# Performance work log

Hardware: AMD Instinct MI355X
Metric: run time of the kernel (lower is better)

## Reference

```python
import jax, jax.numpy as jnp
import numpy as np

INNER = 256   # inner_channel
NODES = 64    # nodes_num (prototypes)
EM_NUM = 3
DIAG_C = 128  # hardcoded diag_channel in FullyConnectGCLayer


def setup_inputs() -> dict:
    key = jax.random.key(0)
    ks = jax.random.split(key, 16)
    b, c, w, h = 4, 1024, 64, 64
    f32 = jnp.float32
    d = {}
    d["x"] = jax.random.normal(ks[0], (b, c, w, h), f32)
    # Conv2d weights re-initialized to N(0, 0.001) in Intra_graph.__init__
    d["W_in"] = 0.001 * jax.random.normal(ks[1], (INNER, c), f32)
    d["b_in"] = jnp.zeros((INNER,), f32)
    d["multi_proto"] = 0.001 * jax.random.normal(ks[2], (1, INNER, NODES), f32)
    d["pi0"] = jnp.ones((1, NODES), f32) / NODES
    # Conv1d layers keep default kaiming-uniform-ish init
    lim = 1.0 / np.sqrt(INNER)
    d["W_adj"] = jax.random.uniform(ks[3], (DIAG_C, INNER), f32, -lim, lim)
    d["b_adj"] = jax.random.uniform(ks[4], (DIAG_C,), f32, -lim, lim)
    d["W_diag"] = jax.random.uniform(ks[5], (DIAG_C, INNER), f32, -lim, lim)
    d["b_diag"] = jax.random.uniform(ks[6], (DIAG_C,), f32, -lim, lim)
    d["gcn_weight"] = 0.01 * jax.random.normal(ks[7], (INNER, INNER), f32)
    d["W_out"] = 0.001 * jax.random.normal(ks[8], (c, INNER), f32)
    d["b_out"] = jnp.zeros((c,), f32)
    d["gamma"] = jnp.ones((c,), f32)
    d["beta"] = jnp.zeros((c,), f32)
    d["W_out2"] = 0.001 * jax.random.normal(ks[9], (c, INNER), f32)
    d["b_out2"] = jnp.zeros((c,), f32)
    d["gamma2"] = jnp.ones((c,), f32)
    d["beta2"] = jnp.zeros((c,), f32)
    d["flag"] = 0
    return d


def _bn(y, g, bt):
    # BatchNorm2d in training mode: batch stats over (N,H,W), biased var, eps=1e-5
    m = jnp.mean(y, (0, 2, 3), keepdims=True)
    v = jnp.var(y, (0, 2, 3), keepdims=True)
    return (y - m) * jax.lax.rsqrt(v + 1e-5) * g[None, :, None, None] + bt[None, :, None, None]


def _forward(x, W_in, b_in, multi_proto, pi0, W_adj, b_adj, W_diag, b_diag,
             gcn_weight, W_out, b_out, gamma, beta, W_out2, b_out2, gamma2, beta2):
    b, c, w, h = x.shape
    wh = w * h
    x1 = (jnp.einsum('oi,bihw->bohw', W_in, x) + b_in[None, :, None, None]).reshape(b, INNER, wh)
    # ---- EM soft-clustering loop (runs under no_grad in torch) ----
    x1s = jax.lax.stop_gradient(x1)
    mu = jnp.broadcast_to(multi_proto, (b, INNER, NODES))
    pi = jnp.broadcast_to(pi0[None, :, :], (b, 1, NODES))
    for _ in range(EM_NUM):
        lik = jnp.einsum('bcm,bcn->bmn', x1s, mu)              # [b, wh, n]
        lik = jnp.exp(lik - jnp.max(lik, 2, keepdims=True))
        post = lik * pi
        post = post / (1e-18 + jnp.sum(post, 2, keepdims=True))
        prob = post / (1e-18 + jnp.sum(post, 1, keepdims=True))
        mu = jnp.einsum('bcm,bmn->bcn', x1s, prob)
        pi = jnp.sum(post, 1, keepdims=True) / wh
    post = jax.lax.stop_gradient(post)
    prob = jax.lax.stop_gradient(prob)
    # ---- aggregate to prototypes (grad flows through x1 only) ----
    x2 = jnp.einsum('bcm,bmn->bcn', x1, prob)                   # [b, inner, n]
    # ---- branch 2: scatter back, conv, bn ----
    x4 = jnp.einsum('bcn,bmn->bcm', x2, post).reshape(b, INNER, w, h)
    x4 = _bn(jnp.einsum('oi,bihw->bohw', W_out2, x4) + b_out2[None, :, None, None], gamma2, beta2)
    output2 = jax.nn.relu(jax.nn.relu(x4) + x)
    # ---- FullyConnectGCLayer on x2 ----
    xd = jnp.einsum('oi,bin->bon', W_diag, x2) + b_diag[None, :, None]
    dvec = jax.nn.sigmoid(jnp.mean(xd, 2))                      # [b, 128]
    xa = jnp.einsum('oi,bin->bon', W_adj, x2) + b_adj[None, :, None]  # [b, 128, n]
    # sigmoid(diag(d)) has 0.5 off-diagonal, sigmoid(d) on diagonal:
    # xa^T S xa = 0.5 * (1^T xa)^T (1^T xa) + xa^T diag(sig(d)-0.5) xa
    u = jnp.sum(xa, 1)                                          # [b, n]
    A = 0.5 * u[:, :, None] * u[:, None, :] + jnp.einsum('bcn,bc,bcm->bnm', xa, dvec - 0.5, xa)
    A = jax.nn.relu(A) + jnp.eye(NODES, dtype=x.dtype)[None]
    deg = jax.lax.stop_gradient(jnp.sum(A, 1) ** -0.5)          # no_grad degree, [b, n]
    A = deg[:, :, None] * A * deg[:, None, :]
    gout = jnp.einsum('oi,bin->bon', gcn_weight, jnp.einsum('bcn,bnm->bcm', x2, A))
    x2g = jax.nn.relu(gout) + x2                                # res_connect
    # ---- branch 1: scatter back, conv, bn ----
    x3 = jnp.einsum('bcn,bmn->bcm', x2g, post).reshape(b, INNER, w, h)
    x3 = _bn(jnp.einsum('oi,bihw->bohw', W_out, x3) + b_out[None, :, None, None], gamma, beta)
    output = jax.nn.relu(jax.nn.relu(x3) + x)
    return output, output2


def reference(x, W_in, b_in, multi_proto, pi0, W_adj, b_adj, W_diag, b_diag,
              gcn_weight, W_out, b_out, gamma, beta, W_out2, b_out2, gamma2, beta2, flag):
    # flag only gates a buffer EMA update (no effect on forward outputs)
    return _forward(x, W_in, b_in, multi_proto, pi0, W_adj, b_adj, W_diag, b_diag,
                    gcn_weight, W_out, b_out, gamma, beta, W_out2, b_out2, gamma2, beta2)
```

## Files before the change

kernel.cpp:

```cpp
#include <hip/hip_runtime.h>
#include <math.h>


typedef unsigned short u16;
typedef short s16x8 __attribute__((ext_vector_type(8)));
typedef float f32x4 __attribute__((ext_vector_type(4)));

constexpr int BB  = 4;
constexpr int CH  = 1024;
constexpr int IN  = 256;
constexpr int ND  = 64;
constexpr int WH  = 4096;
constexpr int DCN = 128;
constexpr size_t TOT = (size_t)BB * CH * WH;

__device__ inline u16 f2bf(float f) {
  unsigned u = __float_as_uint(f);
  return (u16)((u + 0x7fffu + ((u >> 16) & 1u)) >> 16);
}
__device__ inline s16x8 ld8(const u16* p) { return *(const s16x8*)p; }
#define MFMA16(a, b, c) __builtin_amdgcn_mfma_f32_16x16x32_bf16(a, b, c, 0, 0, 0)

__global__ void k_init(const float* __restrict__ Win, const float* __restrict__ mp,
                       const float* __restrict__ pi0, u16* __restrict__ Winb,
                       u16* __restrict__ mu_t, float* __restrict__ piw,
                       float* __restrict__ sp) {
  int idx = blockIdx.x * 256 + threadIdx.x;
  if (idx < IN * CH) { Winb[idx] = f2bf(Win[idx]); return; }
  int j = idx - IN * CH;
  if (j < BB * ND * IN) {
    int bb = j >> 14, n = (j >> 8) & 63, c = j & 255;
    mu_t[((size_t)(bb * ND + n)) * IN + c] = f2bf(mp[c * ND + n]);
    return;
  }
  j -= BB * ND * IN;
  if (j < BB * ND) { piw[j] = pi0[j & 63]; return; }
  j -= BB * ND;
  if (j < 3 * BB * ND) sp[j] = 0.f;
}

__global__ __launch_bounds__(512) void k_x1(
    const float* __restrict__ x, const u16* __restrict__ Winb,
    const float* __restrict__ bin, u16* __restrict__ x1, u16* __restrict__ x1t) {
  __shared__ u16 lt[64][40];
  const int t = threadIdx.x, w = t >> 6, lr = t & 15, lg = (t >> 4) & 3;
  const int wc = w & 3, wm = w >> 2;
  const int m0 = blockIdx.x * 64, b = blockIdx.y;
  const int si = t >> 4, sm = (t & 15) * 4;
  const float* xb = x + (size_t)b * CH * WH + m0 + sm;
  f32x4 acc[4][2];
#pragma unroll
  for (int i = 0; i < 4; ++i)
#pragma unroll
    for (int j = 0; j < 2; ++j) acc[i][j] = (f32x4){0.f, 0.f, 0.f, 0.f};
  const u16* wp = Winb + (size_t)(wc * 64 + lr) * CH + lg * 8;

  float4 nxt = *(const float4*)&xb[(size_t)si * WH];
  for (int k0 = 0; k0 < CH; k0 += 32) {
    float4 cur = nxt;
    __syncthreads();
    lt[sm + 0][si] = f2bf(cur.x); lt[sm + 1][si] = f2bf(cur.y);
    lt[sm + 2][si] = f2bf(cur.z); lt[sm + 3][si] = f2bf(cur.w);
    if (k0 + 32 < CH) nxt = *(const float4*)&xb[(size_t)(k0 + 32 + si) * WH];
    __syncthreads();
    s16x8 af[4], bf[2];
#pragma unroll
    for (int i = 0; i < 4; ++i) af[i] = ld8(wp + (size_t)i * 16 * CH + k0);
#pragma unroll
    for (int j = 0; j < 2; ++j) bf[j] = *(const s16x8*)&lt[wm * 32 + j * 16 + lr][lg * 8];
#pragma unroll
    for (int i = 0; i < 4; ++i)
#pragma unroll
      for (int j = 0; j < 2; ++j) acc[i][j] = MFMA16(af[i], bf[j], acc[i][j]);
  }
#pragma unroll
  for (int i = 0; i < 4; ++i) {
    const int cb = wc * 64 + i * 16 + lg * 4;
    const float4 bi = *(const float4*)&bin[cb];
    const float bia[4] = {bi.x, bi.y, bi.z, bi.w};
#pragma unroll
    for (int j = 0; j < 2; ++j) {
      const int m = m0 + wm * 32 + j * 16 + lr;
      float v[4];
#pragma unroll
      for (int r = 0; r < 4; ++r) v[r] = acc[i][j][r] + bia[r];
      ushort4 o;
      o.x = f2bf(v[0]); o.y = f2bf(v[1]); o.z = f2bf(v[2]); o.w = f2bf(v[3]);
      *(ushort4*)&x1t[((size_t)b * WH + m) * IN + cb] = o;
#pragma unroll
      for (int r = 0; r < 4; ++r)
        x1[((size_t)b * IN + cb + r) * WH + m] = f2bf(v[r]);
    }
  }
}

__global__ __launch_bounds__(256) void k_em(
    const u16* __restrict__ x1, const u16* __restrict__ x1t,
    const u16* __restrict__ mu_t, const float* __restrict__ piw,
    float* __restrict__ sp, u16* __restrict__ pmn,
    float* __restrict__ mup, float* __restrict__ gp, int doLast) {
  __shared__ u16 ptl[64][264];
  const int t = threadIdx.x, w = t >> 6, lr = t & 15, lg = (t >> 4) & 3;
  const int mch = blockIdx.x, b = blockIdx.y;
  const int mbase = mch * 256;
  {
    f32x4 acc[4][4];
#pragma unroll
    for (int i = 0; i < 4; ++i)
#pragma unroll
      for (int f = 0; f < 4; ++f) acc[i][f] = (f32x4){0.f, 0.f, 0.f, 0.f};
    const u16* ap = x1t + ((size_t)b * WH + mbase + w * 64 + lr) * IN + lg * 8;
    const u16* bp = mu_t + ((size_t)b * ND + lr) * IN + lg * 8;
#pragma unroll
    for (int k0 = 0; k0 < IN; k0 += 32) {
      s16x8 bf[4];
#pragma unroll
      for (int f = 0; f < 4; ++f) bf[f] = ld8(bp + f * 16 * IN + k0);
#pragma unroll
      for (int i = 0; i < 4; ++i) {
        s16x8 av = ld8(ap + (size_t)i * 16 * IN + k0);
#pragma unroll
        for (int f = 0; f < 4; ++f) acc[i][f] = MFMA16(av, bf[f], acc[i][f]);
      }
    }
    float pi_[4], spart[4] = {0.f, 0.f, 0.f, 0.f};
#pragma unroll
    for (int f = 0; f < 4; ++f) pi_[f] = piw[b * ND + f * 16 + lr];
#pragma unroll
    for (int i = 0; i < 4; ++i)
#pragma unroll
      for (int r = 0; r < 4; ++r) {
        float v0 = acc[i][0][r], v1 = acc[i][1][r], v2 = acc[i][2][r], v3 = acc[i][3][r];
        float mx = fmaxf(fmaxf(v0, v1), fmaxf(v2, v3));
        mx = fmaxf(mx, __shfl_xor(mx, 1)); mx = fmaxf(mx, __shfl_xor(mx, 2));
        mx = fmaxf(mx, __shfl_xor(mx, 4)); mx = fmaxf(mx, __shfl_xor(mx, 8));
        float e0 = __expf(v0 - mx) * pi_[0], e1 = __expf(v1 - mx) * pi_[1];
        float e2 = __expf(v2 - mx) * pi_[2], e3 = __expf(v3 - mx) * pi_[3];
        float s = e0 + e1 + e2 + e3;
        s += __shfl_xor(s, 1); s += __shfl_xor(s, 2);
        s += __shfl_xor(s, 4); s += __shfl_xor(s, 8);
        const float inv = 1.f / (1e-18f + s);
        e0 *= inv; e1 *= inv; e2 *= inv; e3 *= inv;
        const int mloc = w * 64 + i * 16 + lg * 4 + r;
        u16 q0 = f2bf(e0), q1 = f2bf(e1), q2 = f2bf(e2), q3 = f2bf(e3);
        ptl[0 + lr][mloc]  = q0; ptl[16 + lr][mloc] = q1;
        ptl[32 + lr][mloc] = q2; ptl[48 + lr][mloc] = q3;
        if (doLast) {
          const size_t gbase = ((size_t)b * WH + mbase + mloc) * ND + lr;
          pmn[gbase + 0]  = q0; pmn[gbase + 16] = q1;
          pmn[gbase + 32] = q2; pmn[gbase + 48] = q3;
        }
        spart[0] += e0; spart[1] += e1; spart[2] += e2; spart[3] += e3;
      }
#pragma unroll
    for (int f = 0; f < 4; ++f) {
      spart[f] += __shfl_xor(spart[f], 16);
      spart[f] += __shfl_xor(spart[f], 32);
    }
    if (((t >> 4) & 3) == 0) {
#pragma unroll
      for (int f = 0; f < 4; ++f)
        atomicAdd(&sp[b * ND + f * 16 + lr], spart[f]);
    }
  }
  __syncthreads();
  {
    f32x4 acc[4][4];
#pragma unroll
    for (int i = 0; i < 4; ++i)
#pragma unroll
      for (int j = 0; j < 4; ++j) acc[i][j] = (f32x4){0.f, 0.f, 0.f, 0.f};
    const u16* ap = x1 + ((size_t)b * IN + w * 64 + lr) * WH + mbase + lg * 8;
#pragma unroll
    for (int ks = 0; ks < 8; ++ks) {
      s16x8 af[4], bf[4];
#pragma unroll
      for (int i = 0; i < 4; ++i) af[i] = ld8(ap + (size_t)i * 16 * WH + ks * 32);
#pragma unroll
      for (int j = 0; j < 4; ++j)
        bf[j] = *(const s16x8*)&ptl[j * 16 + lr][ks * 32 + lg * 8];
#pragma unroll
      for (int i = 0; i < 4; ++i)
#pragma unroll
        for (int j = 0; j < 4; ++j) acc[i][j] = MFMA16(af[i], bf[j], acc[i][j]);
    }
    float* mo = mup + ((size_t)mch * BB + b) * (IN * ND);
#pragma unroll
    for (int i = 0; i < 4; ++i)
#pragma unroll
      for (int j = 0; j < 4; ++j)
#pragma unroll
        for (int r = 0; r < 4; ++r) {
          const int c = w * 64 + i * 16 + lg * 4 + r, n = j * 16 + lr;
          mo[c * ND + n] = acc[i][j][r];
        }
  }
  if (doLast) {
    f32x4 acc[4];
#pragma unroll
    for (int j = 0; j < 4; ++j) acc[j] = (f32x4){0.f, 0.f, 0.f, 0.f};
#pragma unroll
    for (int ks = 0; ks < 8; ++ks) {
      s16x8 av = *(const s16x8*)&ptl[w * 16 + lr][ks * 32 + lg * 8];
#pragma unroll
      for (int j = 0; j < 4; ++j) {
        s16x8 bq = *(const s16x8*)&ptl[j * 16 + lr][ks * 32 + lg * 8];
        acc[j] = MFMA16(av, bq, acc[j]);
      }
    }
    float* go = gp + ((size_t)mch * BB + b) * (ND * ND);
#pragma unroll
    for (int j = 0; j < 4; ++j)
#pragma unroll
      for (int r = 0; r < 4; ++r) {
        const int n1 = w * 16 + lg * 4 + r, n2 = j * 16 + lr;
        go[n1 * ND + n2] = acc[j][r];
      }
  }
}

__global__ void k_mu_red(const float* __restrict__ mup, const float* __restrict__ spb,
                         float* __restrict__ piw, float* __restrict__ mu,
                         u16* __restrict__ mu_t, const float* __restrict__ gp,
                         float* __restrict__ G, int doG) {
  const int idx = blockIdx.x * 256 + threadIdx.x;
  const int bb = idx >> 14, c = (idx >> 6) & 255, n = idx & 63;
  float s = 0.f;
#pragma unroll
  for (int ch = 0; ch < 16; ++ch)
    s += mup[((size_t)ch * BB + bb) * (IN * ND) + (idx & 16383)];
  const float v = s / (1e-18f + spb[bb * ND + n]);
  mu[idx] = v;
  mu_t[((size_t)(bb * ND + n)) * IN + c] = f2bf(v);
  if (idx < BB * ND) piw[idx] = spb[idx] * (1.f / (float)WH);
  if (doG && idx < BB * ND * ND) {
    float g = 0.f;
#pragma unroll
    for (int ch = 0; ch < 16; ++ch) g += gp[(size_t)ch * (BB * ND * ND) + idx];
    G[idx] = g;
  }
}

__device__ void zg_body(const float* __restrict__ W, const float* __restrict__ v,
                        float* __restrict__ z, u16* __restrict__ zb,
                        int o0, int bb, int t, char* smem) {
  float (*As)[68] = (float(*)[68])smem;
  float (*Bs)[64] = (float(*)[64])(smem + 4352);
  const int tx = t & 15, ty = t >> 4;
  const int aoo = t >> 2, akq = (t & 3) * 4;
  const int bkk = t >> 4, bnq = (t & 15) * 4;
  float acc[4][4] = {};
  for (int k0 = 0; k0 < IN; k0 += 16) {
    {
      float4 w4 = *(const float4*)&W[(size_t)(o0 + aoo) * IN + k0 + akq];
      As[akq + 0][aoo] = w4.x; As[akq + 1][aoo] = w4.y;
      As[akq + 2][aoo] = w4.z; As[akq + 3][aoo] = w4.w;
    }
    *(float4*)&Bs[bkk][bnq] = *(const float4*)&v[((size_t)bb * IN + k0 + bkk) * ND + bnq];
    __syncthreads();
#pragma unroll
    for (int kk = 0; kk < 16; ++kk) {
      float4 a4 = *(const float4*)&As[kk][ty * 4];
      float4 b4 = *(const float4*)&Bs[kk][tx * 4];
      float ar[4] = {a4.x, a4.y, a4.z, a4.w}, br[4] = {b4.x, b4.y, b4.z, b4.w};
#pragma unroll
      for (int i = 0; i < 4; ++i)
#pragma unroll
        for (int j = 0; j < 4; ++j) acc[i][j] += ar[i] * br[j];
    }
    __syncthreads();
  }
#pragma unroll
  for (int i = 0; i < 4; ++i) {
    float4 r = make_float4(acc[i][0], acc[i][1], acc[i][2], acc[i][3]);
    const size_t off = ((size_t)bb * CH + o0 + ty * 4 + i) * ND + tx * 4;
    *(float4*)&z[off] = r;
    ushort4 h;
    h.x = f2bf(r.x); h.y = f2bf(r.y); h.z = f2bf(r.z); h.w = f2bf(r.w);
    *(ushort4*)&zb[off] = h;
  }
}

__global__ __launch_bounds__(256) void k_gcAz2(
    const float* __restrict__ mu, const float* __restrict__ gw,
    const float* __restrict__ Wa, const float* __restrict__ ba,
    const float* __restrict__ Wd, const float* __restrict__ bd,
    float* __restrict__ qbuf, float* __restrict__ xabuf, float* __restrict__ dv,
    const float* __restrict__ Wo2, float* __restrict__ z2, u16* __restrict__ zb2) {
  __shared__ __align__(16) char smem[66560];
  const int t = threadIdx.x, bid = blockIdx.x;
  if (bid < 28) {
    const int blk = bid % 7, b = bid / 7;
    float* sx2 = (float*)smem;
    float* srm = (float*)(smem + 65536);
    if (blk < 6) {
      const float* src = mu + (size_t)b * IN * ND;
#pragma unroll
      for (int q4 = 0; q4 < 16; ++q4)
        *(float4*)&sx2[q4 * 1024 + t * 4] = *(const float4*)&src[q4 * 1024 + t * 4];
      __syncthreads();
      const int rg = t >> 4, cg2 = t & 15;
      const float* W = (blk < 4) ? gw + (size_t)(blk * 64 + rg * 4) * IN
                                 : Wa + (size_t)((blk - 4) * 64 + rg * 4) * IN;
      float acc[4][4] = {};
      for (int i4 = 0; i4 < 64; ++i4) {
        float4 xv[4];
#pragma unroll
        for (int e = 0; e < 4; ++e)
          xv[e] = *(const float4*)&sx2[(i4 * 4 + e) * 64 + cg2 * 4];
#pragma unroll
        for (int rr = 0; rr < 4; ++rr) {
          const float4 w4 = *(const float4*)&W[(size_t)rr * IN + i4 * 4];
          acc[rr][0] += w4.x * xv[0].x + w4.y * xv[1].x + w4.z * xv[2].x + w4.w * xv[3].x;
          acc[rr][1] += w4.x * xv[0].y + w4.y * xv[1].y + w4.z * xv[2].y + w4.w * xv[3].y;
          acc[rr][2] += w4.x * xv[0].z + w4.y * xv[1].z + w4.z * xv[2].z + w4.w * xv[3].z;
          acc[rr][3] += w4.x * xv[0].w + w4.y * xv[1].w + w4.z * xv[2].w + w4.w * xv[3].w;
        }
      }
      if (blk < 4) {
        float* dst = qbuf + (size_t)b * IN * ND + (size_t)(blk * 64 + rg * 4) * ND + cg2 * 4;
#pragma unroll
        for (int rr = 0; rr < 4; ++rr)
          *(float4*)&dst[(size_t)rr * ND] =
              make_float4(acc[rr][0], acc[rr][1], acc[rr][2], acc[rr][3]);
      } else {
        const int xr = (blk - 4) * 64 + rg * 4;
        float* dst = xabuf + (size_t)b * DCN * ND + (size_t)xr * ND + cg2 * 4;
#pragma unroll
        for (int rr = 0; rr < 4; ++rr) {
          const float bv = ba[xr + rr];
          *(float4*)&dst[(size_t)rr * ND] =
              make_float4(acc[rr][0] + bv, acc[rr][1] + bv, acc[rr][2] + bv, acc[rr][3] + bv);
        }
      }
    } else {
      {
        const float* row = mu + (size_t)b * IN * ND + (size_t)t * ND;
        float s = 0.f;
#pragma unroll
        for (int n4 = 0; n4 < 16; ++n4) {
          float4 v = *(const float4*)&row[n4 * 4];
          s += v.x + v.y + v.z + v.w;
        }
        srm[t] = s * (1.f / ND);
      }
      __syncthreads();
      if (t < DCN) {
        float av = 0.f;
#pragma unroll
        for (int i4 = 0; i4 < 64; ++i4) {
          float4 w4 = *(const float4*)&Wd[(size_t)t * IN + i4 * 4];
          float4 r4 = *(const float4*)&srm[i4 * 4];
          av += w4.x * r4.x + w4.y * r4.y + w4.z * r4.z + w4.w * r4.w;
        }
        av += bd[t];
        dv[b * DCN + t] = 1.f / (1.f + __expf(-av)) - 0.5f;
      }
    }
  } else if (bid >= 32 && bid < 96) {
    const int zid = bid - 32;
    zg_body(Wo2, mu, z2, zb2, (zid & 15) * 64, zid >> 4, t, smem);
  }
}

__global__ __launch_bounds__(256) void k_gcBC(
    const float* __restrict__ xabuf, const float* __restrict__ dv,
    const float* __restrict__ qbuf, const float* __restrict__ mu,
    float* __restrict__ x2g) {
  __shared__ float sxa[DCN * ND];
  __shared__ float sA[ND * 65];
  __shared__ float sq[64 * 68];
  __shared__ float sdv[DCN];
  __shared__ float su[ND];
  __shared__ float sdeg[ND];
  const int t = threadIdx.x, qtr = blockIdx.x, b = blockIdx.y;
  {
    const float* src = xabuf + (size_t)b * DCN * ND;
#pragma unroll
    for (int q4 = 0; q4 < 8; ++q4)
      *(float4*)&sxa[q4 * 1024 + t * 4] = *(const float4*)&src[q4 * 1024 + t * 4];
    if (t < DCN) sdv[t] = dv[b * DCN + t];
    const int r = t >> 2, seg = (t & 3) * 16;
    const float* qs = qbuf + (size_t)b * IN * ND + (size_t)(qtr * 64 + r) * ND + seg;
#pragma unroll
    for (int f = 0; f < 4; ++f) {
      float4 v = *(const float4*)&qs[f * 4];
      sq[r * 68 + seg + f * 4 + 0] = v.x; sq[r * 68 + seg + f * 4 + 1] = v.y;
      sq[r * 68 + seg + f * 4 + 2] = v.z; sq[r * 68 + seg + f * 4 + 3] = v.w;
    }
  }
  __syncthreads();
  if (t < ND) {
    float s = 0.f;
    for (int dc = 0; dc < DCN; ++dc) s += sxa[dc * ND + t];
    su[t] = s;
  }
  __syncthreads();
  {
    const int n1g = t >> 4, n2g = t & 15;
    float acc[4][4] = {};
    for (int dc = 0; dc < DCN; ++dc) {
      const float dvv = sdv[dc];
      float4 v1 = *(const float4*)&sxa[dc * ND + n1g * 4];
      const float4 v2 = *(const float4*)&sxa[dc * ND + n2g * 4];
      v1.x *= dvv; v1.y *= dvv; v1.z *= dvv; v1.w *= dvv;
      acc[0][0] += v1.x * v2.x; acc[0][1] += v1.x * v2.y;
      acc[0][2] += v1.x * v2.z; acc[0][3] += v1.x * v2.w;
      acc[1][0] += v1.y * v2.x; acc[1][1] += v1.y * v2.y;
      acc[1][2] += v1.y * v2.z; acc[1][3] += v1.y * v2.w;
      acc[2][0] += v1.z * v2.x; acc[2][1] += v1.z * v2.y;
      acc[2][2] += v1.z * v2.z; acc[2][3] += v1.z * v2.w;
      acc[3][0] += v1.w * v2.x; acc[3][1] += v1.w * v2.y;
      acc[3][2] += v1.w * v2.z; acc[3][3] += v1.w * v2.w;
    }
#pragma unroll
    for (int i = 0; i < 4; ++i) {
      const int n1 = n1g * 4 + i;
      const float u1 = su[n1];
#pragma unroll
      for (int j = 0; j < 4; ++j) {
        const int n2 = n2g * 4 + j;
        const float v = acc[i][j] + 0.5f * u1 * su[n2];
        sA[n1 * 65 + n2] = fmaxf(v, 0.f) + (n1 == n2 ? 1.f : 0.f);
      }
    }
  }
  __syncthreads();
  if (t < ND) {
    float s = 0.f;
    for (int m = 0; m < ND; ++m) s += sA[m * 65 + t];
    sdeg[t] = rsqrtf(s);
  }
  __syncthreads();
  {
    const int n1g = t >> 4, n2g = t & 15;
#pragma unroll
    for (int i = 0; i < 4; ++i) {
      const int n1 = n1g * 4 + i;
      const float dr = sdeg[n1];
#pragma unroll
      for (int e = 0; e < 4; ++e)
        sA[n1 * 65 + n2g * 4 + e] *= dr * sdeg[n2g * 4 + e];
    }
  }
  __syncthreads();
  {
    const int rg = t >> 4, cg2 = t & 15;
    float acc[4][4] = {};
    for (int k = 0; k < ND; ++k) {
      const float4 a4 = *(const float4*)&sA[k * 65 + cg2 * 4];
      float qv[4];
#pragma unroll
      for (int rr = 0; rr < 4; ++rr) qv[rr] = sq[(rg * 4 + rr) * 68 + k];
#pragma unroll
      for (int rr = 0; rr < 4; ++rr) {
        acc[rr][0] += qv[rr] * a4.x; acc[rr][1] += qv[rr] * a4.y;
        acc[rr][2] += qv[rr] * a4.z; acc[rr][3] += qv[rr] * a4.w;
      }
    }
#pragma unroll
    for (int rr = 0; rr < 4; ++rr) {
      const size_t off = (size_t)b * IN * ND + (size_t)(qtr * 64 + rg * 4 + rr) * ND + cg2 * 4;
      const float4 xv = *(const float4*)&mu[off];
      float4 o;
      o.x = fmaxf(acc[rr][0], 0.f) + xv.x; o.y = fmaxf(acc[rr][1], 0.f) + xv.y;
      o.z = fmaxf(acc[rr][2], 0.f) + xv.z; o.w = fmaxf(acc[rr][3], 0.f) + xv.w;
      *(float4*)&x2g[off] = o;
    }
  }
}

__global__ __launch_bounds__(256) void k_zg(
    const float* __restrict__ W, const float* __restrict__ v,
    float* __restrict__ z, u16* __restrict__ zb) {
  __shared__ __align__(16) char smem[8448];
  zg_body(W, v, z, zb, blockIdx.x * 64, blockIdx.y, threadIdx.x, smem);
}

__global__ __launch_bounds__(256) void k_stats(
    const float* __restrict__ z1, const float* __restrict__ z2,
    const float* __restrict__ sp, const float* __restrict__ G,
    const float* __restrict__ gam, const float* __restrict__ bet,
    const float* __restrict__ gam2, const float* __restrict__ bet2,
    float* __restrict__ abc) {
  const int t = threadIdx.x;
  const int o = blockIdx.x * 4 + (t >> 6), lane = t & 63;
#pragma unroll
  for (int br = 0; br < 2; ++br) {
    const float* z = br ? z2 : z1;
    float macc = 0.f, eacc = 0.f;
    for (int bb = 0; bb < BB; ++bb) {
      const float zv = z[((size_t)bb * CH + o) * ND + lane];
      float s1 = zv * sp[bb * ND + lane];
      const float* Gb = G + (size_t)bb * ND * ND;
      float gz = 0.f;
      for (int k = 0; k < ND; ++k) {
        const float zk = __shfl(zv, k);
        gz += Gb[k * ND + lane] * zk;
      }
      float q = zv * gz;
#pragma unroll
      for (int off = 32; off; off >>= 1) {
        s1 += __shfl_xor(s1, off);
        q  += __shfl_xor(q, off);
      }
      macc += s1; eacc += q;
    }
    const float inv = 1.f / (float)((size_t)BB * WH);
    const float mean = macc * inv;
    const float var  = eacc * inv - mean * mean;
    const float a = (br ? gam2[o] : gam[o]) * rsqrtf(var + 1e-5f);
    const float c = (br ? bet2[o] : bet[o]) - mean * a;
    if (lane == 0) { abc[br * 2 * CH + o] = a; abc[br * 2 * CH + CH + o] = c; }
  }
}

__global__ __launch_bounds__(256) void k_epi(
    const u16* __restrict__ zb1, const u16* __restrict__ zb2,
    const u16* __restrict__ post, const float* __restrict__ abc,
    const float* __restrict__ x, float* __restrict__ out1, float* __restrict__ out2) {
  const int t = threadIdx.x, w = t >> 6, lr = t & 15, lg = (t >> 4) & 3;
  const int m0 = blockIdx.x * 256 + w * 64, o0 = blockIdx.y * 64, bb = blockIdx.z;
  f32x4 acc1[4][4], acc2[4][4];
#pragma unroll
  for (int i = 0; i < 4; ++i)
#pragma unroll
    for (int j = 0; j < 4; ++j) {
      acc1[i][j] = (f32x4){0.f, 0.f, 0.f, 0.f};
      acc2[i][j] = (f32x4){0.f, 0.f, 0.f, 0.f};
    }
  const u16* z1p = zb1 + ((size_t)bb * CH + o0 + lr) * ND + lg * 8;
  const u16* z2p = zb2 + ((size_t)bb * CH + o0 + lr) * ND + lg * 8;
  const u16* pp  = post + ((size_t)bb * WH + m0 + lr) * ND + lg * 8;
#pragma unroll
  for (int ks = 0; ks < 2; ++ks) {
    s16x8 a1[4], a2[4], bq[4];
#pragma unroll
    for (int i = 0; i < 4; ++i) {
      a1[i] = ld8(z1p + i * 16 * ND + ks * 32);
      a2[i] = ld8(z2p + i * 16 * ND + ks * 32);
    }
#pragma unroll
    for (int j = 0; j < 4; ++j) bq[j] = ld8(pp + j * 16 * ND + ks * 32);
#pragma unroll
    for (int i = 0; i < 4; ++i)
#pragma unroll
      for (int j = 0; j < 4; ++j) {
        acc1[i][j] = MFMA16(a1[i], bq[j], acc1[i][j]);
        acc2[i][j] = MFMA16(a2[i], bq[j], acc2[i][j]);
      }
  }
#pragma unroll
  for (int i = 0; i < 4; ++i)
#pragma unroll
    for (int r = 0; r < 4; ++r) {
      const int o = o0 + i * 16 + lg * 4 + r;
      const float a1v = abc[o], c1v = abc[CH + o];
      const float a2v = abc[2 * CH + o], c2v = abc[3 * CH + o];
      const size_t base = ((size_t)bb * CH + o) * WH + m0 + lr;
#pragma unroll
      for (int j = 0; j < 4; ++j) {
        const size_t off = base + j * 16;
        const float xv = __builtin_nontemporal_load(&x[off]);
        const float r1 = fmaxf(fmaxf(a1v * acc1[i][j][r] + c1v, 0.f) + xv, 0.f);
        const float r2 = fmaxf(fmaxf(a2v * acc2[i][j][r] + c2v, 0.f) + xv, 0.f);
        __builtin_nontemporal_store(r1, &out1[off]);
        __builtin_nontemporal_store(r2, &out2[off]);
      }
    }
}

extern "C" void kernel_launch(void* const* d_in, const int* in_sizes, int n_in,
                              void* d_out, int out_size, void* d_ws, size_t ws_size,
                              hipStream_t stream) {
  (void)in_sizes; (void)n_in; (void)out_size; (void)ws_size;
  const float* x    = (const float*)d_in[0];
  const float* Win  = (const float*)d_in[1];
  const float* bin  = (const float*)d_in[2];
  const float* mp   = (const float*)d_in[3];
  const float* pi0  = (const float*)d_in[4];
  const float* Wa   = (const float*)d_in[5];
  const float* ba   = (const float*)d_in[6];
  const float* Wd   = (const float*)d_in[7];
  const float* bd   = (const float*)d_in[8];
  const float* gw   = (const float*)d_in[9];
  const float* Wo   = (const float*)d_in[10];
  const float* gam  = (const float*)d_in[12];
  const float* bet  = (const float*)d_in[13];
  const float* Wo2  = (const float*)d_in[14];
  const float* gam2 = (const float*)d_in[16];
  const float* bet2 = (const float*)d_in[17];

  char* ob = (char*)d_out;
  char* wp = (char*)d_ws;
  float* mup = (float*)(ob + 0);
  float* gp  = (float*)(ob + 4194304);
  float* z1  = (float*)(ob + 5242880);
  float* z2  = (float*)(ob + 6291456);
  u16*   x1    = (u16*)(wp + 0);
  u16*   x1t   = (u16*)(wp + 8388608);
  u16*   Winb  = (u16*)(wp + 16777216);
  u16*   mu_t  = (u16*)(wp + 17301504);
  u16*   pmn   = (u16*)(wp + 17432576);
  float* mu    = (float*)(wp + 19529728);
  float* x2g   = (float*)(wp + 19791872);
  u16*   zb1   = (u16*)(wp + 20054016);
  u16*   zb2   = (u16*)(wp + 20578304);
  float* sp3   = (float*)(wp + 21102592);
  float* piw   = (float*)(wp + 21105664);
  float* abc   = (float*)(wp + 21106688);
  float* G     = (float*)(wp + 21123072);
  float* qbuf  = (float*)(wp + 21188608);
  float* xabuf = (float*)(wp + 21450752);
  float* dvb   = (float*)(wp + 21581824);
  float* out1  = (float*)d_out;
  float* out2  = out1 + TOT;

  k_init<<<dim3(1284), 256, 0, stream>>>(Win, mp, pi0, Winb, mu_t, piw, sp3);
  k_x1<<<dim3(64, BB), 512, 0, stream>>>(x, Winb, bin, x1, x1t);
  for (int it = 0; it < 3; ++it) {
    float* spb = sp3 + it * 256;
    const int doLast = (it == 2);
    k_em<<<dim3(16, BB), 256, 0, stream>>>(x1, x1t, mu_t, piw, spb, pmn, mup, gp, doLast);
    k_mu_red<<<dim3(256), 256, 0, stream>>>(mup, spb, piw, mu, mu_t, gp, G, doLast);
  }
  k_gcAz2<<<dim3(96), 256, 0, stream>>>(mu, gw, Wa, ba, Wd, bd, qbuf, xabuf, dvb,
                                        Wo2, z2, zb2);
  k_gcBC<<<dim3(4, BB), 256, 0, stream>>>(xabuf, dvb, qbuf, mu, x2g);
  k_zg<<<dim3(16, BB), 256, 0, stream>>>(Wo, x2g, z1, zb1);
  k_stats<<<dim3(256), 256, 0, stream>>>(z1, z2, sp3 + 512, G, gam, bet, gam2, bet2, abc);
  k_epi<<<dim3(16, 16, BB), 256, 0, stream>>>(zb1, zb2, pmn, abc, x, out1, out2);
}
```

Measured before the change: 276.5 us.

## Fuse EM mu reduction into k_em via atomics and spread over more blocks

Removes the separate k_mu_red kernel. k_em now accumulates mu and G directly with float atomics into per-iteration buffers, and the next iteration or the downstream kernels apply the 1/sum normalisation on load. The EM grid grows from 16x4 to 64x4 blocks with 64-pixel chunks, and mu is staged in LDS as bf16 inside each block, so occupancy should rise and three launches disappear. In exchange there are many more global float atomics (each block adds a 256x64 tile), summation order becomes nondeterministic, and the normalisation is recomputed redundantly in several consumers.

```diff
diff --git a/kernel.cpp b/kernel.cpp
--- a/kernel.cpp
+++ b/kernel.cpp
@@ -22,21 +22,18 @@
 #define MFMA16(a, b, c) __builtin_amdgcn_mfma_f32_16x16x32_bf16(a, b, c, 0, 0, 0)
 
 __global__ void k_init(const float* __restrict__ Win, const float* __restrict__ mp,
-                       const float* __restrict__ pi0, u16* __restrict__ Winb,
-                       u16* __restrict__ mu_t, float* __restrict__ piw,
-                       float* __restrict__ sp) {
+                       u16* __restrict__ Winb, float* __restrict__ macc,
+                       float* __restrict__ spbuf, float* __restrict__ G) {
   int idx = blockIdx.x * 256 + threadIdx.x;
   if (idx < IN * CH) { Winb[idx] = f2bf(Win[idx]); return; }
   int j = idx - IN * CH;
-  if (j < BB * ND * IN) {
-    int bb = j >> 14, n = (j >> 8) & 63, c = j & 255;
-    mu_t[((size_t)(bb * ND + n)) * IN + c] = f2bf(mp[c * ND + n]);
-    return;
-  }
-  j -= BB * ND * IN;
-  if (j < BB * ND) { piw[j] = pi0[j & 63]; return; }
-  j -= BB * ND;
-  if (j < 3 * BB * ND) sp[j] = 0.f;
+  if (j < BB * IN * ND) { macc[j] = mp[j & (IN * ND - 1)]; return; }
+  j -= BB * IN * ND;
+  if (j < 3 * BB * IN * ND) { macc[BB * IN * ND + j] = 0.f; return; }
+  j -= 3 * BB * IN * ND;
+  if (j < 4 * BB * ND) { spbuf[j] = 0.f; return; }
+  j -= 4 * BB * ND;
+  if (j < BB * ND * ND) G[j] = 0.f;
 }
 
 __global__ __launch_bounds__(512) void k_x1(
@@ -96,62 +93,74 @@
 
 __global__ __launch_bounds__(256) void k_em(
     const u16* __restrict__ x1, const u16* __restrict__ x1t,
-    const u16* __restrict__ mu_t, const float* __restrict__ piw,
-    float* __restrict__ sp, u16* __restrict__ pmn,
-    float* __restrict__ mup, float* __restrict__ gp, int doLast) {
-  __shared__ u16 ptl[64][264];
+    const float* __restrict__ maccPrev, const float* __restrict__ spPrev,
+    const float* __restrict__ pi0, float* __restrict__ maccNext,
+    float* __restrict__ spNext, u16* __restrict__ pmn, float* __restrict__ G,
+    int it0, int doLast) {
+  __shared__ u16 lt_mu[64][264];
+  __shared__ u16 ptl[64][72];
   const int t = threadIdx.x, w = t >> 6, lr = t & 15, lg = (t >> 4) & 3;
   const int mch = blockIdx.x, b = blockIdx.y;
-  const int mbase = mch * 256;
   {
-    f32x4 acc[4][4];
-#pragma unroll
-    for (int i = 0; i < 4; ++i)
-#pragma unroll
-      for (int f = 0; f < 4; ++f) acc[i][f] = (f32x4){0.f, 0.f, 0.f, 0.f};
-    const u16* ap = x1t + ((size_t)b * WH + mbase + w * 64 + lr) * IN + lg * 8;
-    const u16* bp = mu_t + ((size_t)b * ND + lr) * IN + lg * 8;
+    const int n0 = (t * 4) & 63;
+    float inv[4];
+#pragma unroll
+    for (int e = 0; e < 4; ++e)
+      inv[e] = it0 ? 1.f : 1.f / (1e-18f + spPrev[b * ND + n0 + e]);
+    const float* src = maccPrev + (size_t)b * (IN * ND);
+#pragma unroll
+    for (int q = 0; q < 16; ++q) {
+      const int idx = q * 1024 + t * 4;
+      const int c = idx >> 6;
+      float4 v = *(const float4*)&src[idx];
+      lt_mu[n0 + 0][c] = f2bf(v.x * inv[0]);
+      lt_mu[n0 + 1][c] = f2bf(v.y * inv[1]);
+      lt_mu[n0 + 2][c] = f2bf(v.z * inv[2]);
+      lt_mu[n0 + 3][c] = f2bf(v.w * inv[3]);
+    }
+  }
+  __syncthreads();
+  {
+    f32x4 acc[4];
+#pragma unroll
+    for (int f = 0; f < 4; ++f) acc[f] = (f32x4){0.f, 0.f, 0.f, 0.f};
+    const u16* ap = x1t + ((size_t)b * WH + mch * 64 + w * 16 + lr) * IN + lg * 8;
 #pragma unroll
     for (int k0 = 0; k0 < IN; k0 += 32) {
-      s16x8 bf[4];
-#pragma unroll
-      for (int f = 0; f < 4; ++f) bf[f] = ld8(bp + f * 16 * IN + k0);
-#pragma unroll
-      for (int i = 0; i < 4; ++i) {
-        s16x8 av = ld8(ap + (size_t)i * 16 * IN + k0);
-#pragma unroll
-        for (int f = 0; f < 4; ++f) acc[i][f] = MFMA16(av, bf[f], acc[i][f]);
-      }
+      s16x8 av = ld8(ap + k0);
+#pragma unroll
+      for (int f = 0; f < 4; ++f)
+        acc[f] = MFMA16(av, *(const s16x8*)&lt_mu[f * 16 + lr][lg * 8 + k0], acc[f]);
     }
     float pi_[4], spart[4] = {0.f, 0.f, 0.f, 0.f};
 #pragma unroll
-    for (int f = 0; f < 4; ++f) pi_[f] = piw[b * ND + f * 16 + lr];
-#pragma unroll
-    for (int i = 0; i < 4; ++i)
-#pragma unroll
-      for (int r = 0; r < 4; ++r) {
-        float v0 = acc[i][0][r], v1 = acc[i][1][r], v2 = acc[i][2][r], v3 = acc[i][3][r];
-        float mx = fmaxf(fmaxf(v0, v1), fmaxf(v2, v3));
-        mx = fmaxf(mx, __shfl_xor(mx, 1)); mx = fmaxf(mx, __shfl_xor(mx, 2));
-        mx = fmaxf(mx, __shfl_xor(mx, 4)); mx = fmaxf(mx, __shfl_xor(mx, 8));
-        float e0 = __expf(v0 - mx) * pi_[0], e1 = __expf(v1 - mx) * pi_[1];
-        float e2 = __expf(v2 - mx) * pi_[2], e3 = __expf(v3 - mx) * pi_[3];
-        float s = e0 + e1 + e2 + e3;
-        s += __shfl_xor(s, 1); s += __shfl_xor(s, 2);
-        s += __shfl_xor(s, 4); s += __shfl_xor(s, 8);
-        const float inv = 1.f / (1e-18f + s);
-        e0 *= inv; e1 *= inv; e2 *= inv; e3 *= inv;
-        const int mloc = w * 64 + i * 16 + lg * 4 + r;
-        u16 q0 = f2bf(e0), q1 = f2bf(e1), q2 = f2bf(e2), q3 = f2bf(e3);
-        ptl[0 + lr][mloc]  = q0; ptl[16 + lr][mloc] = q1;
-        ptl[32 + lr][mloc] = q2; ptl[48 + lr][mloc] = q3;
-        if (doLast) {
-          const size_t gbase = ((size_t)b * WH + mbase + mloc) * ND + lr;
-          pmn[gbase + 0]  = q0; pmn[gbase + 16] = q1;
-          pmn[gbase + 32] = q2; pmn[gbase + 48] = q3;
-        }
-        spart[0] += e0; spart[1] += e1; spart[2] += e2; spart[3] += e3;
-      }
+    for (int f = 0; f < 4; ++f)
+      pi_[f] = it0 ? pi0[f * 16 + lr]
+                   : spPrev[b * ND + f * 16 + lr] * (1.f / (float)WH);
+#pragma unroll
+    for (int r = 0; r < 4; ++r) {
+      float v0 = acc[0][r], v1 = acc[1][r], v2 = acc[2][r], v3 = acc[3][r];
+      float mx = fmaxf(fmaxf(v0, v1), fmaxf(v2, v3));
+      mx = fmaxf(mx, __shfl_xor(mx, 1)); mx = fmaxf(mx, __shfl_xor(mx, 2));
+      mx = fmaxf(mx, __shfl_xor(mx, 4)); mx = fmaxf(mx, __shfl_xor(mx, 8));
+      float e0 = __expf(v0 - mx) * pi_[0], e1 = __expf(v1 - mx) * pi_[1];
+      float e2 = __expf(v2 - mx) * pi_[2], e3 = __expf(v3 - mx) * pi_[3];
+      float s = e0 + e1 + e2 + e3;
+      s += __shfl_xor(s, 1); s += __shfl_xor(s, 2);
+      s += __shfl_xor(s, 4); s += __shfl_xor(s, 8);
+      const float inv = 1.f / (1e-18f + s);
+      e0 *= inv; e1 *= inv; e2 *= inv; e3 *= inv;
+      const int mloc = w * 16 + lg * 4 + r;
+      u16 q0 = f2bf(e0), q1 = f2bf(e1), q2 = f2bf(e2), q3 = f2bf(e3);
+      ptl[0 + lr][mloc]  = q0; ptl[16 + lr][mloc] = q1;
+      ptl[32 + lr][mloc] = q2; ptl[48 + lr][mloc] = q3;
+      if (doLast) {
+        const size_t gbase = ((size_t)b * WH + mch * 64 + mloc) * ND + lr;
+        pmn[gbase + 0]  = q0; pmn[gbase + 16] = q1;
+        pmn[gbase + 32] = q2; pmn[gbase + 48] = q3;
+      }
+      spart[0] += e0; spart[1] += e1; spart[2] += e2; spart[3] += e3;
+    }
 #pragma unroll
     for (int f = 0; f < 4; ++f) {
       spart[f] += __shfl_xor(spart[f], 16);
@@ -160,7 +169,7 @@
     if (((t >> 4) & 3) == 0) {
 #pragma unroll
       for (int f = 0; f < 4; ++f)
-        atomicAdd(&sp[b * ND + f * 16 + lr], spart[f]);
+        atomicAdd(&spNext[b * ND + f * 16 + lr], spart[f]);
     }
   }
   __syncthreads();
@@ -170,9 +179,9 @@
     for (int i = 0; i < 4; ++i)
 #pragma unroll
       for (int j = 0; j < 4; ++j) acc[i][j] = (f32x4){0.f, 0.f, 0.f, 0.f};
-    const u16* ap = x1 + ((size_t)b * IN + w * 64 + lr) * WH + mbase + lg * 8;
-#pragma unroll
-    for (int ks = 0; ks < 8; ++ks) {
+    const u16* ap = x1 + ((size_t)b * IN + w * 64 + lr) * WH + mch * 64 + lg * 8;
+#pragma unroll
+    for (int ks = 0; ks < 2; ++ks) {
       s16x8 af[4], bf[4];
 #pragma unroll
       for (int i = 0; i < 4; ++i) af[i] = ld8(ap + (size_t)i * 16 * WH + ks * 32);
@@ -184,7 +193,7 @@
 #pragma unroll
         for (int j = 0; j < 4; ++j) acc[i][j] = MFMA16(af[i], bf[j], acc[i][j]);
     }
-    float* mo = mup + ((size_t)mch * BB + b) * (IN * ND);
+    float* mo = maccNext + (size_t)b * (IN * ND);
 #pragma unroll
     for (int i = 0; i < 4; ++i)
 #pragma unroll
@@ -192,7 +201,7 @@
 #pragma unroll
         for (int r = 0; r < 4; ++r) {
           const int c = w * 64 + i * 16 + lg * 4 + r, n = j * 16 + lr;
-          mo[c * ND + n] = acc[i][j][r];
+          atomicAdd(&mo[c * ND + n], acc[i][j][r]);
         }
   }
   if (doLast) {
@@ -200,7 +209,7 @@
 #pragma unroll
     for (int j = 0; j < 4; ++j) acc[j] = (f32x4){0.f, 0.f, 0.f, 0.f};
 #pragma unroll
-    for (int ks = 0; ks < 8; ++ks) {
+    for (int ks = 0; ks < 2; ++ks) {
       s16x8 av = *(const s16x8*)&ptl[w * 16 + lr][ks * 32 + lg * 8];
 #pragma unroll
       for (int j = 0; j < 4; ++j) {
@@ -208,47 +217,31 @@
         acc[j] = MFMA16(av, bq, acc[j]);
       }
     }
-    float* go = gp + ((size_t)mch * BB + b) * (ND * ND);
+    float* go = G + (size_t)b * (ND * ND);
 #pragma unroll
     for (int j = 0; j < 4; ++j)
 #pragma unroll
       for (int r = 0; r < 4; ++r) {
         const int n1 = w * 16 + lg * 4 + r, n2 = j * 16 + lr;
-        go[n1 * ND + n2] = acc[j][r];
-      }
-  }
-}
-
-__global__ void k_mu_red(const float* __restrict__ mup, const float* __restrict__ spb,
-                         float* __restrict__ piw, float* __restrict__ mu,
-                         u16* __restrict__ mu_t, const float* __restrict__ gp,
-                         float* __restrict__ G, int doG) {
-  const int idx = blockIdx.x * 256 + threadIdx.x;
-  const int bb = idx >> 14, c = (idx >> 6) & 255, n = idx & 63;
-  float s = 0.f;
-#pragma unroll
-  for (int ch = 0; ch < 16; ++ch)
-    s += mup[((size_t)ch * BB + bb) * (IN * ND) + (idx & 16383)];
-  const float v = s / (1e-18f + spb[bb * ND + n]);
-  mu[idx] = v;
-  mu_t[((size_t)(bb * ND + n)) * IN + c] = f2bf(v);
-  if (idx < BB * ND) piw[idx] = spb[idx] * (1.f / (float)WH);
-  if (doG && idx < BB * ND * ND) {
-    float g = 0.f;
-#pragma unroll
-    for (int ch = 0; ch < 16; ++ch) g += gp[(size_t)ch * (BB * ND * ND) + idx];
-    G[idx] = g;
+        atomicAdd(&go[n1 * ND + n2], acc[j][r]);
+      }
   }
 }
 
 __device__ void zg_body(const float* __restrict__ W, const float* __restrict__ v,
                         float* __restrict__ z, u16* __restrict__ zb,
-                        int o0, int bb, int t, char* smem) {
+                        int o0, int bb, int t, char* smem,
+                        const float* __restrict__ spn) {
   float (*As)[68] = (float(*)[68])smem;
   float (*Bs)[64] = (float(*)[64])(smem + 4352);
   const int tx = t & 15, ty = t >> 4;
   const int aoo = t >> 2, akq = (t & 3) * 4;
   const int bkk = t >> 4, bnq = (t & 15) * 4;
+  float inv4[4] = {1.f, 1.f, 1.f, 1.f};
+  if (spn) {
+#pragma unroll
+    for (int e = 0; e < 4; ++e) inv4[e] = 1.f / (1e-18f + spn[bb * ND + bnq + e]);
+  }
   float acc[4][4] = {};
   for (int k0 = 0; k0 < IN; k0 += 16) {
     {
@@ -256,7 +249,11 @@
       As[akq + 0][aoo] = w4.x; As[akq + 1][aoo] = w4.y;
       As[akq + 2][aoo] = w4.z; As[akq + 3][aoo] = w4.w;
     }
-    *(float4*)&Bs[bkk][bnq] = *(const float4*)&v[((size_t)bb * IN + k0 + bkk) * ND + bnq];
+    {
+      float4 bv = *(const float4*)&v[((size_t)bb * IN + k0 + bkk) * ND + bnq];
+      Bs[bkk][bnq + 0] = bv.x * inv4[0]; Bs[bkk][bnq + 1] = bv.y * inv4[1];
+      Bs[bkk][bnq + 2] = bv.z * inv4[2]; Bs[bkk][bnq + 3] = bv.w * inv4[3];
+    }
     __syncthreads();
 #pragma unroll
     for (int kk = 0; kk < 16; ++kk) {
@@ -282,22 +279,34 @@
 }
 
 __global__ __launch_bounds__(256) void k_gcAz2(
-    const float* __restrict__ mu, const float* __restrict__ gw,
-    const float* __restrict__ Wa, const float* __restrict__ ba,
-    const float* __restrict__ Wd, const float* __restrict__ bd,
-    float* __restrict__ qbuf, float* __restrict__ xabuf, float* __restrict__ dv,
+    const float* __restrict__ macc3, const float* __restrict__ spL,
+    const float* __restrict__ gw, const float* __restrict__ Wa,
+    const float* __restrict__ ba, const float* __restrict__ Wd,
+    const float* __restrict__ bd, float* __restrict__ qbuf,
+    float* __restrict__ xabuf, float* __restrict__ dv,
     const float* __restrict__ Wo2, float* __restrict__ z2, u16* __restrict__ zb2) {
   __shared__ __align__(16) char smem[66560];
   const int t = threadIdx.x, bid = blockIdx.x;
   if (bid < 28) {
     const int blk = bid % 7, b = bid / 7;
-    float* sx2 = (float*)smem;
-    float* srm = (float*)(smem + 65536);
     if (blk < 6) {
-      const float* src = mu + (size_t)b * IN * ND;
-#pragma unroll
-      for (int q4 = 0; q4 < 16; ++q4)
-        *(float4*)&sx2[q4 * 1024 + t * 4] = *(const float4*)&src[q4 * 1024 + t * 4];
+      float* sx2 = (float*)smem;
+      const float* src = macc3 + (size_t)b * IN * ND;
+      {
+        const int n0 = (t * 4) & 63;
+        float inv4[4];
+#pragma unroll
+        for (int e = 0; e < 4; ++e)
+          inv4[e] = 1.f / (1e-18f + spL[b * ND + n0 + e]);
+#pragma unroll
+        for (int q4 = 0; q4 < 16; ++q4) {
+          float4 v = *(const float4*)&src[q4 * 1024 + t * 4];
+          sx2[q4 * 1024 + t * 4 + 0] = v.x * inv4[0];
+          sx2[q4 * 1024 + t * 4 + 1] = v.y * inv4[1];
+          sx2[q4 * 1024 + t * 4 + 2] = v.z * inv4[2];
+          sx2[q4 * 1024 + t * 4 + 3] = v.w * inv4[3];
+        }
+      }
       __syncthreads();
       const int rg = t >> 4, cg2 = t & 15;
       const float* W = (blk < 4) ? gw + (size_t)(blk * 64 + rg * 4) * IN
@@ -334,13 +343,18 @@
         }
       }
     } else {
+      float* sinv = (float*)smem;
+      float* srm  = (float*)(smem + 1024);
+      if (t < ND) sinv[t] = 1.f / (1e-18f + spL[b * ND + t]);
+      __syncthreads();
       {
-        const float* row = mu + (size_t)b * IN * ND + (size_t)t * ND;
+        const float* row = macc3 + (size_t)b * IN * ND + (size_t)t * ND;
         float s = 0.f;
 #pragma unroll
         for (int n4 = 0; n4 < 16; ++n4) {
           float4 v = *(const float4*)&row[n4 * 4];
-          s += v.x + v.y + v.z + v.w;
+          s += v.x * sinv[n4 * 4 + 0] + v.y * sinv[n4 * 4 + 1] +
+               v.z * sinv[n4 * 4 + 2] + v.w * sinv[n4 * 4 + 3];
         }
         srm[t] = s * (1.f / ND);
       }
@@ -359,14 +373,14 @@
     }
   } else if (bid >= 32 && bid < 96) {
     const int zid = bid - 32;
-    zg_body(Wo2, mu, z2, zb2, (zid & 15) * 64, zid >> 4, t, smem);
+    zg_body(Wo2, macc3, z2, zb2, (zid & 15) * 64, zid >> 4, t, smem, spL);
   }
 }
 
 __global__ __launch_bounds__(256) void k_gcBC(
     const float* __restrict__ xabuf, const float* __restrict__ dv,
-    const float* __restrict__ qbuf, const float* __restrict__ mu,
-    float* __restrict__ x2g) {
+    const float* __restrict__ qbuf, const float* __restrict__ macc3,
+    const float* __restrict__ spL, float* __restrict__ x2g) {
   __shared__ float sxa[DCN * ND];
   __shared__ float sA[ND * 65];
   __shared__ float sq[64 * 68];
@@ -446,6 +460,10 @@
   __syncthreads();
   {
     const int rg = t >> 4, cg2 = t & 15;
+    float inv4[4];
+#pragma unroll
+    for (int e = 0; e < 4; ++e)
+      inv4[e] = 1.f / (1e-18f + spL[b * ND + cg2 * 4 + e]);
     float acc[4][4] = {};
     for (int k = 0; k < ND; ++k) {
       const float4 a4 = *(const float4*)&sA[k * 65 + cg2 * 4];
@@ -461,10 +479,12 @@
 #pragma unroll
     for (int rr = 0; rr < 4; ++rr) {
       const size_t off = (size_t)b * IN * ND + (size_t)(qtr * 64 + rg * 4 + rr) * ND + cg2 * 4;
-      const float4 xv = *(const float4*)&mu[off];
+      const float4 xv = *(const float4*)&macc3[off];
       float4 o;
-      o.x = fmaxf(acc[rr][0], 0.f) + xv.x; o.y = fmaxf(acc[rr][1], 0.f) + xv.y;
-      o.z = fmaxf(acc[rr][2], 0.f) + xv.z; o.w = fmaxf(acc[rr][3], 0.f) + xv.w;
+      o.x = fmaxf(acc[rr][0], 0.f) + xv.x * inv4[0];
+      o.y = fmaxf(acc[rr][1], 0.f) + xv.y * inv4[1];
+      o.z = fmaxf(acc[rr][2], 0.f) + xv.z * inv4[2];
+      o.w = fmaxf(acc[rr][3], 0.f) + xv.w * inv4[3];
       *(float4*)&x2g[off] = o;
     }
   }
@@ -474,7 +494,7 @@
     const float* __restrict__ W, const float* __restrict__ v,
     float* __restrict__ z, u16* __restrict__ zb) {
   __shared__ __align__(16) char smem[8448];
-  zg_body(W, v, z, zb, blockIdx.x * 64, blockIdx.y, threadIdx.x, smem);
+  zg_body(W, v, z, zb, blockIdx.x * 64, blockIdx.y, threadIdx.x, smem, nullptr);
 }
 
 __global__ __launch_bounds__(256) void k_stats(
@@ -593,41 +613,40 @@
 
   char* ob = (char*)d_out;
   char* wp = (char*)d_ws;
-  float* mup = (float*)(ob + 0);
-  float* gp  = (float*)(ob + 4194304);
-  float* z1  = (float*)(ob + 5242880);
-  float* z2  = (float*)(ob + 6291456);
+  float* z1 = (float*)(ob + 0);
+  float* z2 = (float*)(ob + 1048576);
   u16*   x1    = (u16*)(wp + 0);
   u16*   x1t   = (u16*)(wp + 8388608);
   u16*   Winb  = (u16*)(wp + 16777216);
-  u16*   mu_t  = (u16*)(wp + 17301504);
-  u16*   pmn   = (u16*)(wp + 17432576);
-  float* mu    = (float*)(wp + 19529728);
-  float* x2g   = (float*)(wp + 19791872);
-  u16*   zb1   = (u16*)(wp + 20054016);
-  u16*   zb2   = (u16*)(wp + 20578304);
-  float* sp3   = (float*)(wp + 21102592);
-  float* piw   = (float*)(wp + 21105664);
-  float* abc   = (float*)(wp + 21106688);
-  float* G     = (float*)(wp + 21123072);
-  float* qbuf  = (float*)(wp + 21188608);
-  float* xabuf = (float*)(wp + 21450752);
-  float* dvb   = (float*)(wp + 21581824);
+  u16*   pmn   = (u16*)(wp + 17301504);
+  float* macc  = (float*)(wp + 19398656);
+  float* spbuf = (float*)(wp + 20447232);
+  float* G     = (float*)(wp + 20451328);
+  float* qbuf  = (float*)(wp + 20516864);
+  float* xabuf = (float*)(wp + 20779008);
+  float* dvb   = (float*)(wp + 20910080);
+  float* x2g   = (float*)(wp + 20912128);
+  u16*   zb1   = (u16*)(wp + 21174272);
+  u16*   zb2   = (u16*)(wp + 21698560);
+  float* abc   = (float*)(wp + 22222848);
   float* out1  = (float*)d_out;
   float* out2  = out1 + TOT;
 
-  k_init<<<dim3(1284), 256, 0, stream>>>(Win, mp, pi0, Winb, mu_t, piw, sp3);
+  float* macc3 = macc + 3 * (BB * IN * ND);
+  float* spL   = spbuf + 3 * (BB * ND);
+
+  k_init<<<dim3(2116), 256, 0, stream>>>(Win, mp, Winb, macc, spbuf, G);
   k_x1<<<dim3(64, BB), 512, 0, stream>>>(x, Winb, bin, x1, x1t);
   for (int it = 0; it < 3; ++it) {
-    float* spb = sp3 + it * 256;
-    const int doLast = (it == 2);
-    k_em<<<dim3(16, BB), 256, 0, stream>>>(x1, x1t, mu_t, piw, spb, pmn, mup, gp, doLast);
-    k_mu_red<<<dim3(256), 256, 0, stream>>>(mup, spb, piw, mu, mu_t, gp, G, doLast);
-  }
-  k_gcAz2<<<dim3(96), 256, 0, stream>>>(mu, gw, Wa, ba, Wd, bd, qbuf, xabuf, dvb,
-                                        Wo2, z2, zb2);
-  k_gcBC<<<dim3(4, BB), 256, 0, stream>>>(xabuf, dvb, qbuf, mu, x2g);
+    k_em<<<dim3(64, BB), 256, 0, stream>>>(
+        x1, x1t, macc + it * (BB * IN * ND), spbuf + it * (BB * ND), pi0,
+        macc + (it + 1) * (BB * IN * ND), spbuf + (it + 1) * (BB * ND),
+        pmn, G, it == 0 ? 1 : 0, it == 2 ? 1 : 0);
+  }
+  k_gcAz2<<<dim3(96), 256, 0, stream>>>(macc3, spL, gw, Wa, ba, Wd, bd,
+                                        qbuf, xabuf, dvb, Wo2, z2, zb2);
+  k_gcBC<<<dim3(4, BB), 256, 0, stream>>>(xabuf, dvb, qbuf, macc3, spL, x2g);
   k_zg<<<dim3(16, BB), 256, 0, stream>>>(Wo, x2g, z1, zb1);
-  k_stats<<<dim3(256), 256, 0, stream>>>(z1, z2, sp3 + 512, G, gam, bet, gam2, bet2, abc);
+  k_stats<<<dim3(256), 256, 0, stream>>>(z1, z2, spL, G, gam, bet, gam2, bet2, abc);
   k_epi<<<dim3(16, 16, BB), 256, 0, stream>>>(zb1, zb2, pmn, abc, x, out1, out2);
 }
```

Measured after the change: 289.7 us. +4.8%, slower.
